# Performance work log

Measured on AMD Instinct MI355X. Metric: run time of the kernel, lower is better.

Reference implementation:

```python
import jax, jax.numpy as jnp
import numpy as np

N = 100000   # nodes
E = 1600000  # edges (avg degree 16)
D = 128      # in = hid = out dim
EPS = 1e-5   # BatchNorm eps


def setup_inputs() -> dict:
    key = jax.random.key(0)
    ks = jax.random.split(key, 14)
    x = jax.random.normal(ks[0], (N, D), dtype=jnp.float32)
    row = jax.random.randint(ks[1], (E,), 0, N, dtype=jnp.int32)
    col = jax.random.randint(ks[2], (E,), 0, N, dtype=jnp.int32)
    edge_weight = jax.random.uniform(ks[3], (E,), dtype=jnp.float32)
    s = 1.0 / np.sqrt(D)
    W0 = jax.random.uniform(ks[4], (D, D), jnp.float32, -s, s)
    b0 = jax.random.uniform(ks[5], (D,), jnp.float32, -s, s)
    W1 = jax.random.uniform(ks[6], (D, D), jnp.float32, -s, s)
    b1 = jax.random.uniform(ks[7], (D,), jnp.float32, -s, s)
    W2 = jax.random.uniform(ks[8], (D, D), jnp.float32, -s, s)
    b2 = jax.random.uniform(ks[9], (D,), jnp.float32, -s, s)
    g0 = jnp.ones((D,), jnp.float32); be0 = jnp.zeros((D,), jnp.float32)
    g1 = jnp.ones((D,), jnp.float32); be1 = jnp.zeros((D,), jnp.float32)
    return {"x": x, "edge_weight": edge_weight,
            "W0": W0, "b0": b0, "g0": g0, "be0": be0,
            "W1": W1, "b1": b1, "g1": g1, "be1": be1,
            "W2": W2, "b2": b2, "row": row, "col": col}


def _spmm(edge_weight, row, col, h):
    # (A_norm @ h) with A in COO: out[r] = sum_e w_e * h[col_e] for row_e == r
    return jax.ops.segment_sum(edge_weight[:, None] * h[col], row, num_segments=N)


def _bn(h, gamma, beta):
    # BatchNorm1d, training-mode stats (biased variance), over the node axis
    m = h.mean(axis=0)
    v = h.var(axis=0)
    return gamma * (h - m) * jax.lax.rsqrt(v + EPS) + beta


def reference(x, edge_weight, W0, b0, g0, be0, W1, b1, g1, be1, W2, b2, row, col):
    # hidden block 1: SpMM(A, Linear(h)) -> BN -> ReLU (dropout p=0)
    h = jax.nn.relu(_bn(_spmm(edge_weight, row, col, x @ W0 + b0), g0, be0))
    # hidden block 2
    h = jax.nn.relu(_bn(_spmm(edge_weight, row, col, h @ W1 + b1), g1, be1))
    # final layer: SpMM(A, Linear(h)), no BN/activation
    return _spmm(edge_weight, row, col, h @ W2 + b2)
```

## Files before the change

### kernel.cpp

```cpp
#include <hip/hip_runtime.h>
#include <cstddef>

#define DD 128
#define EPS 1e-5f

typedef short short8 __attribute__((ext_vector_type(8)));
typedef float float4v __attribute__((ext_vector_type(4)));

__device__ __forceinline__ unsigned short f2bf(float f) {
    union { float f; unsigned int u; } x; x.f = f;
    unsigned int r = x.u + 0x7fffu + ((x.u >> 16) & 1u);
    return (unsigned short)(r >> 16);
}
__device__ __forceinline__ float bfhi2f(unsigned int hi_bits) {
    union { unsigned int u; float f; } x; x.u = hi_bits;
    return x.f;
}


__global__ void hist_kernel(const int* __restrict__ row, int* __restrict__ deg, int E) {
    int e = blockIdx.x * blockDim.x + threadIdx.x;
    if (e < E) atomicAdd(&deg[row[e]], 1);
}

__global__ void scanA_kernel(const int* __restrict__ deg, int* __restrict__ tmp,
                             int* __restrict__ bsum, int n) {
    __shared__ int s[1024];
    int tid = threadIdx.x;
    int gid = blockIdx.x * 1024 + tid;
    int v = (gid < n) ? deg[gid] : 0;
    s[tid] = v;
    __syncthreads();
    for (int off = 1; off < 1024; off <<= 1) {
        int t = s[tid];
        int u = (tid >= off) ? s[tid - off] : 0;
        __syncthreads();
        s[tid] = t + u;
        __syncthreads();
    }
    if (gid < n) tmp[gid] = s[tid];
    if (tid == 1023) bsum[blockIdx.x] = s[1023];
}

__global__ void scanB_kernel(const int* __restrict__ bsum, int* __restrict__ boff,
                             int* __restrict__ row_start, int nb, int n) {
    __shared__ int s[128];
    int tid = threadIdx.x;
    int v = (tid < nb) ? bsum[tid] : 0;
    s[tid] = v;
    __syncthreads();
    for (int off = 1; off < 128; off <<= 1) {
        int t = s[tid];
        int u = (tid >= off) ? s[tid - off] : 0;
        __syncthreads();
        s[tid] = t + u;
        __syncthreads();
    }
    if (tid < nb) boff[tid] = s[tid] - v;
    if (tid == nb - 1) row_start[n] = s[tid];
}

__global__ void scanC_kernel(const int* __restrict__ deg, const int* __restrict__ tmp,
                             const int* __restrict__ boff, int* __restrict__ row_start,
                             int* __restrict__ cursor, int n) {
    int gid = blockIdx.x * 1024 + threadIdx.x;
    if (gid < n) {
        int rs = tmp[gid] - deg[gid] + boff[blockIdx.x];
        row_start[gid] = rs;
        cursor[gid] = rs;
    }
}

#define SCHUNK 2048

__global__ __launch_bounds__(256) void scatter_bucketed_kernel(
    const int* __restrict__ row, const int* __restrict__ col,
    const float* __restrict__ ew, int* __restrict__ cursor,
    unsigned long long* __restrict__ ebuf, int E, unsigned int bmagic) {
    int chunk = blockIdx.x >> 3;
    unsigned int bucket = blockIdx.x & 7;
    int base = chunk * SCHUNK + threadIdx.x;
    #pragma unroll
    for (int i = 0; i < SCHUNK / 256; ++i) {
        int e = base + i * 256;
        if (e < E) {
            int r = row[e];
            if (__umulhi((unsigned int)r, bmagic) == bucket) {
                int p = atomicAdd(&cursor[r], 1);
                unsigned long long pk = (unsigned long long)(unsigned int)col[e]
                                      | ((unsigned long long)__float_as_uint(ew[e]) << 32);
                ebuf[p] = pk;
            }
        }
    }
}


__global__ void convw_kernel(const float* __restrict__ W0, const float* __restrict__ W1,
                             const float* __restrict__ W2, unsigned short* __restrict__ T0,
                             unsigned short* __restrict__ T1, unsigned short* __restrict__ T2) {
    const float* W = (blockIdx.y == 0) ? W0 : (blockIdx.y == 1) ? W1 : W2;
    unsigned short* T = (blockIdx.y == 0) ? T0 : (blockIdx.y == 1) ? T1 : T2;
    int gid = blockIdx.x * 256 + threadIdx.x;
    int k = gid >> 7, n = gid & 127;
    T[n * DD + k] = f2bf(W[k * DD + n]);
}


__global__ __launch_bounds__(256) void gemm_mfma_kernel(
    const float* __restrict__ A, const unsigned short* __restrict__ Wt,
    const float* __restrict__ bias,
    const float* __restrict__ sums, const float* __restrict__ g,
    const float* __restrict__ be,
    int doBN, unsigned short* __restrict__ H, int nrows)
{
    __shared__ unsigned short Asl[64][136];
    __shared__ unsigned short Wsl[128][136];
    __shared__ float scl_s[128], sft_s[128];

    const int tid  = threadIdx.x;
    const int row0 = blockIdx.x * 64;

    if (doBN && tid < 128) {
        float inv_n = 1.0f / (float)nrows;
        float mean = sums[tid] * inv_n;
        float var = sums[128 + tid] * inv_n - mean * mean;
        float rstd = rsqrtf(var + EPS);
        float sc = g[tid] * rstd;
        scl_s[tid] = sc;
        sft_s[tid] = be[tid] - mean * sc;
    }
    if (doBN) __syncthreads();

    for (int i = tid; i < 2048; i += 256) {
        int r = i >> 4, off = (i & 15) * 8;
        *(uint4*)&Wsl[r][off] = *(const uint4*)(Wt + (size_t)r * DD + off);
    }
    for (int i = tid; i < 2048; i += 256) {
        int r = i >> 5, off4 = i & 31;
        int grow = row0 + r;
        float4 v = make_float4(0.f, 0.f, 0.f, 0.f);
        if (grow < nrows)
            v = *(const float4*)(A + (size_t)grow * DD + off4 * 4);
        if (doBN) {
            float4 sc = *(const float4*)&scl_s[off4 * 4];
            float4 sh = *(const float4*)&sft_s[off4 * 4];
            v.x = fmaxf(0.f, v.x * sc.x + sh.x);
            v.y = fmaxf(0.f, v.y * sc.y + sh.y);
            v.z = fmaxf(0.f, v.z * sc.z + sh.z);
            v.w = fmaxf(0.f, v.w * sc.w + sh.w);
        }
        ushort4 p;
        p.x = f2bf(v.x); p.y = f2bf(v.y); p.z = f2bf(v.z); p.w = f2bf(v.w);
        *(ushort4*)&Asl[r][off4 * 4] = p;
    }
    __syncthreads();

    const int w = tid >> 6, lane = tid & 63;
    const int m = lane & 15, q = lane >> 4;

    short8 afr[4];
    #pragma unroll
    for (int c = 0; c < 4; ++c)
        afr[c] = *(const short8*)&Asl[w * 16 + m][c * 32 + q * 8];

    float4v acc[8];
    #pragma unroll
    for (int t = 0; t < 8; ++t) acc[t] = (float4v){0.f, 0.f, 0.f, 0.f};

    #pragma unroll
    for (int t = 0; t < 8; ++t) {
        #pragma unroll
        for (int c = 0; c < 4; ++c) {
            short8 bfr = *(const short8*)&Wsl[t * 16 + m][c * 32 + q * 8];
            acc[t] = __builtin_amdgcn_mfma_f32_16x16x32_bf16(afr[c], bfr, acc[t], 0, 0, 0);
        }
    }

    #pragma unroll
    for (int t = 0; t < 8; ++t) {
        float bv = bias[t * 16 + m];
        #pragma unroll
        for (int i = 0; i < 4; ++i)
            Asl[w * 16 + q * 4 + i][t * 16 + m] = f2bf(acc[t][i] + bv);
    }
    __syncthreads();

    for (int i = tid; i < 1024; i += 256) {
        int r = i >> 4, off = (i & 15) * 8;
        if (row0 + r < nrows)
            *(uint4*)(H + (size_t)(row0 + r) * DD + off) = *(const uint4*)&Asl[r][off];
    }
}


__global__ __launch_bounds__(256) void spmm_bf16_kernel(
    const unsigned short* __restrict__ H, const int* __restrict__ row_start,
    const unsigned long long* __restrict__ ebuf,
    float* __restrict__ S, int N)
{
    int g = threadIdx.x >> 6, lane = threadIdx.x & 63;
    int r = blockIdx.x * 4 + g;
    if (r >= N) return;
    int e0 = row_start[r];
    int e1 = row_start[r + 1];
    float ax = 0.f, ay = 0.f;
    const unsigned short* Hp = H + lane * 2;
    int e = e0;
    for (; e + 3 < e1; e += 4) {
        unsigned long long p0 = __builtin_nontemporal_load(&ebuf[e]);
        unsigned long long p1 = __builtin_nontemporal_load(&ebuf[e + 1]);
        unsigned long long p2 = __builtin_nontemporal_load(&ebuf[e + 2]);
        unsigned long long p3 = __builtin_nontemporal_load(&ebuf[e + 3]);
        unsigned int u0 = *(const unsigned int*)(Hp + (size_t)(unsigned int)p0 * DD);
        unsigned int u1 = *(const unsigned int*)(Hp + (size_t)(unsigned int)p1 * DD);
        unsigned int u2 = *(const unsigned int*)(Hp + (size_t)(unsigned int)p2 * DD);
        unsigned int u3 = *(const unsigned int*)(Hp + (size_t)(unsigned int)p3 * DD);
        float w0 = __uint_as_float((unsigned int)(p0 >> 32));
        float w1 = __uint_as_float((unsigned int)(p1 >> 32));
        float w2 = __uint_as_float((unsigned int)(p2 >> 32));
        float w3 = __uint_as_float((unsigned int)(p3 >> 32));
        ax += w0 * bfhi2f(u0 << 16);
        ay += w0 * bfhi2f(u0 & 0xffff0000u);
        ax += w1 * bfhi2f(u1 << 16);
        ay += w1 * bfhi2f(u1 & 0xffff0000u);
        ax += w2 * bfhi2f(u2 << 16);
        ay += w2 * bfhi2f(u2 & 0xffff0000u);
        ax += w3 * bfhi2f(u3 << 16);
        ay += w3 * bfhi2f(u3 & 0xffff0000u);
    }
    for (; e < e1; ++e) {
        unsigned long long p0 = __builtin_nontemporal_load(&ebuf[e]);
        unsigned int u0 = *(const unsigned int*)(Hp + (size_t)(unsigned int)p0 * DD);
        float w0 = __uint_as_float((unsigned int)(p0 >> 32));
        ax += w0 * bfhi2f(u0 << 16);
        ay += w0 * bfhi2f(u0 & 0xffff0000u);
    }
    float2 o; o.x = ax; o.y = ay;
    *(float2*)(S + (size_t)r * DD + lane * 2) = o;
}


__global__ void bn_stats_kernel(const float* __restrict__ S, float* __restrict__ sums, int n) {
    __shared__ float ls[256], ls2[256];
    int tid = threadIdx.x;
    int c = tid & 127;
    float s = 0.f, s2 = 0.f;
    size_t total = (size_t)n * DD;
    #pragma unroll 8
    for (size_t i = (size_t)blockIdx.x * 256 + tid; i < total; i += (size_t)256 * 256) {
        float v = S[i];
        s += v;
        s2 += v * v;
    }
    ls[tid] = s;
    ls2[tid] = s2;
    __syncthreads();
    if (tid < 128) {
        s  = ls[tid] + ls[tid + 128];
        s2 = ls2[tid] + ls2[tid + 128];
        atomicAdd(&sums[c], s);
        atomicAdd(&sums[128 + c], s2);
    }
}


extern "C" void kernel_launch(void* const* d_in, const int* in_sizes, int n_in,
                              void* d_out, int out_size, void* d_ws, size_t ws_size,
                              hipStream_t stream) {
    const float* x   = (const float*)d_in[0];
    const float* ew  = (const float*)d_in[1];
    const float* W0  = (const float*)d_in[2];
    const float* b0  = (const float*)d_in[3];
    const float* g0  = (const float*)d_in[4];
    const float* be0 = (const float*)d_in[5];
    const float* W1  = (const float*)d_in[6];
    const float* b1  = (const float*)d_in[7];
    const float* g1  = (const float*)d_in[8];
    const float* be1 = (const float*)d_in[9];
    const float* W2  = (const float*)d_in[10];
    const float* b2  = (const float*)d_in[11];
    const int* row   = (const int*)d_in[12];
    const int* col   = (const int*)d_in[13];

    const int N = in_sizes[0] / DD;
    const int E = in_sizes[1];
    float* out = (float*)d_out;

    char* w = (char*)d_ws;
    unsigned short* H   = (unsigned short*)w; w += (size_t)N * DD * 2;
    unsigned long long* ebuf = (unsigned long long*)w; w += (size_t)E * 8;
    unsigned short* Wt0 = (unsigned short*)w; w += DD * DD * 2;
    unsigned short* Wt1 = (unsigned short*)w; w += DD * DD * 2;
    unsigned short* Wt2 = (unsigned short*)w; w += DD * DD * 2;
    float* sums         = (float*)w;          w += 256 * 4;
    int*   deg          = (int*)w;            w += (size_t)N * 4;
    int*   tmp          = (int*)w;            w += (size_t)N * 4;
    int*   cursor       = (int*)w;            w += (size_t)N * 4;
    int*   bsum         = (int*)w;            w += 128 * 4;
    int*   boff         = (int*)w;            w += 128 * 4;
    int*   row_start    = (int*)w;            w += (size_t)(N + 1) * 4;

    unsigned int bmagic = (unsigned int)(((unsigned long long)8 << 32) / (unsigned long long)N);

    hipMemsetAsync(deg, 0, (size_t)N * 4, stream);
    hist_kernel<<<(E + 255) / 256, 256, 0, stream>>>(row, deg, E);
    int NB = (N + 1023) / 1024;
    scanA_kernel<<<NB, 1024, 0, stream>>>(deg, tmp, bsum, N);
    scanB_kernel<<<1, 128, 0, stream>>>(bsum, boff, row_start, NB, N);
    scanC_kernel<<<NB, 1024, 0, stream>>>(deg, tmp, boff, row_start, cursor, N);
    int nchunks = (E + SCHUNK - 1) / SCHUNK;
    scatter_bucketed_kernel<<<nchunks * 8, 256, 0, stream>>>(row, col, ew, cursor, ebuf, E, bmagic);

    convw_kernel<<<dim3(64, 3), 256, 0, stream>>>(W0, W1, W2, Wt0, Wt1, Wt2);

    int gblocks = (N + 63) / 64;
    int sblocks = (N + 3) / 4;

    gemm_mfma_kernel<<<gblocks, 256, 0, stream>>>(x, Wt0, b0, nullptr, nullptr, nullptr, 0, H, N);
    spmm_bf16_kernel<<<sblocks, 256, 0, stream>>>(H, row_start, ebuf, out, N);
    hipMemsetAsync(sums, 0, 256 * 4, stream);
    bn_stats_kernel<<<256, 256, 0, stream>>>(out, sums, N);

    gemm_mfma_kernel<<<gblocks, 256, 0, stream>>>(out, Wt1, b1, sums, g0, be0, 1, H, N);
    spmm_bf16_kernel<<<sblocks, 256, 0, stream>>>(H, row_start, ebuf, out, N);
    hipMemsetAsync(sums, 0, 256 * 4, stream);
    bn_stats_kernel<<<256, 256, 0, stream>>>(out, sums, N);

    gemm_mfma_kernel<<<gblocks, 256, 0, stream>>>(out, Wt2, b2, sums, g1, be1, 1, H, N);
    spmm_bf16_kernel<<<sblocks, 256, 0, stream>>>(H, row_start, ebuf, out, N);
}
```

Baseline: 675.8 us.

## Store intermediate SpMM outputs in bf16 and unroll SpMM gather by eight

The first two SpMM layers now write their outputs as packed bf16 instead of fp32, and the BN statistics and the following GEMM read that bf16 buffer. This halves the traffic for the write, the stats pass and the GEMM input load. The GEMM is split into an fp32-input variant and a bf16-input variant with BN fused. The SpMM inner loop is unrolled to eight gathers in flight. The cost is extra rounding of the pre-BN activations to bf16, which slightly changes the BN statistics and the numerics.

```diff
diff --git a/kernel.cpp b/kernel.cpp
--- a/kernel.cpp
+++ b/kernel.cpp
@@ -107,12 +107,76 @@
 }
 
 
-__global__ __launch_bounds__(256) void gemm_mfma_kernel(
+__global__ __launch_bounds__(256) void gemm_mfma_f32_kernel(
     const float* __restrict__ A, const unsigned short* __restrict__ Wt,
+    const float* __restrict__ bias, unsigned short* __restrict__ H, int nrows)
+{
+    __shared__ unsigned short Asl[64][136];
+    __shared__ unsigned short Wsl[128][136];
+
+    const int tid  = threadIdx.x;
+    const int row0 = blockIdx.x * 64;
+
+    for (int i = tid; i < 2048; i += 256) {
+        int r = i >> 4, off = (i & 15) * 8;
+        *(uint4*)&Wsl[r][off] = *(const uint4*)(Wt + (size_t)r * DD + off);
+    }
+    for (int i = tid; i < 2048; i += 256) {
+        int r = i >> 5, off4 = i & 31;
+        int grow = row0 + r;
+        float4 v = make_float4(0.f, 0.f, 0.f, 0.f);
+        if (grow < nrows)
+            v = *(const float4*)(A + (size_t)grow * DD + off4 * 4);
+        ushort4 p;
+        p.x = f2bf(v.x); p.y = f2bf(v.y); p.z = f2bf(v.z); p.w = f2bf(v.w);
+        *(ushort4*)&Asl[r][off4 * 4] = p;
+    }
+    __syncthreads();
+
+    const int w = tid >> 6, lane = tid & 63;
+    const int m = lane & 15, q = lane >> 4;
+
+    short8 afr[4];
+    #pragma unroll
+    for (int c = 0; c < 4; ++c)
+        afr[c] = *(const short8*)&Asl[w * 16 + m][c * 32 + q * 8];
+
+    float4v acc[8];
+    #pragma unroll
+    for (int t = 0; t < 8; ++t) acc[t] = (float4v){0.f, 0.f, 0.f, 0.f};
+
+    #pragma unroll
+    for (int t = 0; t < 8; ++t) {
+        #pragma unroll
+        for (int c = 0; c < 4; ++c) {
+            short8 bfr = *(const short8*)&Wsl[t * 16 + m][c * 32 + q * 8];
+            acc[t] = __builtin_amdgcn_mfma_f32_16x16x32_bf16(afr[c], bfr, acc[t], 0, 0, 0);
+        }
+    }
+
+    #pragma unroll
+    for (int t = 0; t < 8; ++t) {
+        float bv = bias[t * 16 + m];
+        #pragma unroll
+        for (int i = 0; i < 4; ++i)
+            Asl[w * 16 + q * 4 + i][t * 16 + m] = f2bf(acc[t][i] + bv);
+    }
+    __syncthreads();
+
+    for (int i = tid; i < 1024; i += 256) {
+        int r = i >> 4, off = (i & 15) * 8;
+        if (row0 + r < nrows)
+            *(uint4*)(H + (size_t)(row0 + r) * DD + off) = *(const uint4*)&Asl[r][off];
+    }
+}
+
+
+__global__ __launch_bounds__(256) void gemm_mfma_bf16_kernel(
+    const unsigned int* __restrict__ A, const unsigned short* __restrict__ Wt,
     const float* __restrict__ bias,
     const float* __restrict__ sums, const float* __restrict__ g,
     const float* __restrict__ be,
-    int doBN, unsigned short* __restrict__ H, int nrows)
+    unsigned short* __restrict__ H, int nrows)
 {
     __shared__ unsigned short Asl[64][136];
     __shared__ unsigned short Wsl[128][136];
@@ -121,7 +185,7 @@
     const int tid  = threadIdx.x;
     const int row0 = blockIdx.x * 64;
 
-    if (doBN && tid < 128) {
+    if (tid < 128) {
         float inv_n = 1.0f / (float)nrows;
         float mean = sums[tid] * inv_n;
         float var = sums[128 + tid] * inv_n - mean * mean;
@@ -130,29 +194,31 @@
         scl_s[tid] = sc;
         sft_s[tid] = be[tid] - mean * sc;
     }
-    if (doBN) __syncthreads();
 
     for (int i = tid; i < 2048; i += 256) {
         int r = i >> 4, off = (i & 15) * 8;
         *(uint4*)&Wsl[r][off] = *(const uint4*)(Wt + (size_t)r * DD + off);
     }
-    for (int i = tid; i < 2048; i += 256) {
-        int r = i >> 5, off4 = i & 31;
+    __syncthreads();
+
+    for (int i = tid; i < 1024; i += 256) {
+        int r = i >> 4, ch = (i & 15) * 8;
         int grow = row0 + r;
-        float4 v = make_float4(0.f, 0.f, 0.f, 0.f);
+        uint4 u = make_uint4(0, 0, 0, 0);
         if (grow < nrows)
-            v = *(const float4*)(A + (size_t)grow * DD + off4 * 4);
-        if (doBN) {
-            float4 sc = *(const float4*)&scl_s[off4 * 4];
-            float4 sh = *(const float4*)&sft_s[off4 * 4];
-            v.x = fmaxf(0.f, v.x * sc.x + sh.x);
-            v.y = fmaxf(0.f, v.y * sc.y + sh.y);
-            v.z = fmaxf(0.f, v.z * sc.z + sh.z);
-            v.w = fmaxf(0.f, v.w * sc.w + sh.w);
-        }
-        ushort4 p;
-        p.x = f2bf(v.x); p.y = f2bf(v.y); p.z = f2bf(v.z); p.w = f2bf(v.w);
-        *(ushort4*)&Asl[r][off4 * 4] = p;
+            u = *(const uint4*)(A + (size_t)grow * 64 + (ch >> 1));
+        unsigned int uu[4] = {u.x, u.y, u.z, u.w};
+        unsigned int outp[4];
+        #pragma unroll
+        for (int j = 0; j < 4; ++j) {
+            float vx = bfhi2f(uu[j] << 16);
+            float vy = bfhi2f(uu[j] & 0xffff0000u);
+            int k = ch + j * 2;
+            vx = fmaxf(0.f, vx * scl_s[k] + sft_s[k]);
+            vy = fmaxf(0.f, vy * scl_s[k + 1] + sft_s[k + 1]);
+            outp[j] = (unsigned int)f2bf(vx) | ((unsigned int)f2bf(vy) << 16);
+        }
+        *(uint4*)&Asl[r][ch] = *(const uint4*)outp;
     }
     __syncthreads();
 
@@ -197,37 +263,45 @@
 __global__ __launch_bounds__(256) void spmm_bf16_kernel(
     const unsigned short* __restrict__ H, const int* __restrict__ row_start,
     const unsigned long long* __restrict__ ebuf,
-    float* __restrict__ S, int N)
+    float* __restrict__ Sf, unsigned int* __restrict__ Sb, int writeBF, int N)
 {
     int g = threadIdx.x >> 6, lane = threadIdx.x & 63;
     int r = blockIdx.x * 4 + g;
     if (r >= N) return;
-    int e0 = row_start[r];
-    int e1 = row_start[r + 1];
+    int e0 = row_start[r], e1 = row_start[r + 1];
+    const unsigned short* Hp = H + lane * 2;
     float ax = 0.f, ay = 0.f;
-    const unsigned short* Hp = H + lane * 2;
     int e = e0;
-    for (; e + 3 < e1; e += 4) {
-        unsigned long long p0 = __builtin_nontemporal_load(&ebuf[e]);
-        unsigned long long p1 = __builtin_nontemporal_load(&ebuf[e + 1]);
-        unsigned long long p2 = __builtin_nontemporal_load(&ebuf[e + 2]);
-        unsigned long long p3 = __builtin_nontemporal_load(&ebuf[e + 3]);
-        unsigned int u0 = *(const unsigned int*)(Hp + (size_t)(unsigned int)p0 * DD);
-        unsigned int u1 = *(const unsigned int*)(Hp + (size_t)(unsigned int)p1 * DD);
-        unsigned int u2 = *(const unsigned int*)(Hp + (size_t)(unsigned int)p2 * DD);
-        unsigned int u3 = *(const unsigned int*)(Hp + (size_t)(unsigned int)p3 * DD);
-        float w0 = __uint_as_float((unsigned int)(p0 >> 32));
-        float w1 = __uint_as_float((unsigned int)(p1 >> 32));
-        float w2 = __uint_as_float((unsigned int)(p2 >> 32));
-        float w3 = __uint_as_float((unsigned int)(p3 >> 32));
-        ax += w0 * bfhi2f(u0 << 16);
-        ay += w0 * bfhi2f(u0 & 0xffff0000u);
-        ax += w1 * bfhi2f(u1 << 16);
-        ay += w1 * bfhi2f(u1 & 0xffff0000u);
-        ax += w2 * bfhi2f(u2 << 16);
-        ay += w2 * bfhi2f(u2 & 0xffff0000u);
-        ax += w3 * bfhi2f(u3 << 16);
-        ay += w3 * bfhi2f(u3 & 0xffff0000u);
+    for (; e + 7 < e1; e += 8) {
+        unsigned long long p[8];
+        #pragma unroll
+        for (int j = 0; j < 8; ++j) p[j] = __builtin_nontemporal_load(&ebuf[e + j]);
+        unsigned int u[8];
+        #pragma unroll
+        for (int j = 0; j < 8; ++j)
+            u[j] = *(const unsigned int*)(Hp + (size_t)(unsigned int)p[j] * DD);
+        #pragma unroll
+        for (int j = 0; j < 8; ++j) {
+            float wj = __uint_as_float((unsigned int)(p[j] >> 32));
+            ax += wj * bfhi2f(u[j] << 16);
+            ay += wj * bfhi2f(u[j] & 0xffff0000u);
+        }
+    }
+    if (e + 3 < e1) {
+        unsigned long long p[4];
+        #pragma unroll
+        for (int j = 0; j < 4; ++j) p[j] = __builtin_nontemporal_load(&ebuf[e + j]);
+        unsigned int u[4];
+        #pragma unroll
+        for (int j = 0; j < 4; ++j)
+            u[j] = *(const unsigned int*)(Hp + (size_t)(unsigned int)p[j] * DD);
+        #pragma unroll
+        for (int j = 0; j < 4; ++j) {
+            float wj = __uint_as_float((unsigned int)(p[j] >> 32));
+            ax += wj * bfhi2f(u[j] << 16);
+            ay += wj * bfhi2f(u[j] & 0xffff0000u);
+        }
+        e += 4;
     }
     for (; e < e1; ++e) {
         unsigned long long p0 = __builtin_nontemporal_load(&ebuf[e]);
@@ -236,31 +310,41 @@
         ax += w0 * bfhi2f(u0 << 16);
         ay += w0 * bfhi2f(u0 & 0xffff0000u);
     }
-    float2 o; o.x = ax; o.y = ay;
-    *(float2*)(S + (size_t)r * DD + lane * 2) = o;
-}
-
-
-__global__ void bn_stats_kernel(const float* __restrict__ S, float* __restrict__ sums, int n) {
-    __shared__ float ls[256], ls2[256];
+    if (writeBF) {
+        unsigned int pk = (unsigned int)f2bf(ax) | ((unsigned int)f2bf(ay) << 16);
+        Sb[(size_t)r * 64 + lane] = pk;
+    } else {
+        float2 o; o.x = ax; o.y = ay;
+        *(float2*)(Sf + (size_t)r * DD + lane * 2) = o;
+    }
+}
+
+
+__global__ void bn_stats_bf16_kernel(const unsigned int* __restrict__ Sb,
+                                     float* __restrict__ sums, int n) {
+    __shared__ float lsx[256], lsx2[256], lsy[256], lsy2[256];
     int tid = threadIdx.x;
-    int c = tid & 127;
-    float s = 0.f, s2 = 0.f;
-    size_t total = (size_t)n * DD;
-    #pragma unroll 8
-    for (size_t i = (size_t)blockIdx.x * 256 + tid; i < total; i += (size_t)256 * 256) {
-        float v = S[i];
-        s += v;
-        s2 += v * v;
-    }
-    ls[tid] = s;
-    ls2[tid] = s2;
-    __syncthreads();
-    if (tid < 128) {
-        s  = ls[tid] + ls[tid + 128];
-        s2 = ls2[tid] + ls2[tid + 128];
-        atomicAdd(&sums[c], s);
-        atomicAdd(&sums[128 + c], s2);
+    int c2 = tid & 63;
+    float sx = 0.f, sx2 = 0.f, sy = 0.f, sy2 = 0.f;
+    int total = n * 64;
+    for (int i = blockIdx.x * 256 + tid; i < total; i += 256 * 256) {
+        unsigned int u = Sb[i];
+        float vx = bfhi2f(u << 16);
+        float vy = bfhi2f(u & 0xffff0000u);
+        sx += vx; sx2 += vx * vx;
+        sy += vy; sy2 += vy * vy;
+    }
+    lsx[tid] = sx; lsx2[tid] = sx2; lsy[tid] = sy; lsy2[tid] = sy2;
+    __syncthreads();
+    if (tid < 64) {
+        sx  = lsx[tid]  + lsx[tid + 64]  + lsx[tid + 128]  + lsx[tid + 192];
+        sx2 = lsx2[tid] + lsx2[tid + 64] + lsx2[tid + 128] + lsx2[tid + 192];
+        sy  = lsy[tid]  + lsy[tid + 64]  + lsy[tid + 128]  + lsy[tid + 192];
+        sy2 = lsy2[tid] + lsy2[tid + 64] + lsy2[tid + 128] + lsy2[tid + 192];
+        atomicAdd(&sums[2 * c2], sx);
+        atomicAdd(&sums[2 * c2 + 1], sy);
+        atomicAdd(&sums[128 + 2 * c2], sx2);
+        atomicAdd(&sums[129 + 2 * c2], sy2);
     }
 }
 
@@ -289,6 +373,7 @@
 
     char* w = (char*)d_ws;
     unsigned short* H   = (unsigned short*)w; w += (size_t)N * DD * 2;
+    unsigned int* Sb    = (unsigned int*)w;   w += (size_t)N * 64 * 4;
     unsigned long long* ebuf = (unsigned long long*)w; w += (size_t)E * 8;
     unsigned short* Wt0 = (unsigned short*)w; w += DD * DD * 2;
     unsigned short* Wt1 = (unsigned short*)w; w += DD * DD * 2;
@@ -317,16 +402,16 @@
     int gblocks = (N + 63) / 64;
     int sblocks = (N + 3) / 4;
 
-    gemm_mfma_kernel<<<gblocks, 256, 0, stream>>>(x, Wt0, b0, nullptr, nullptr, nullptr, 0, H, N);
-    spmm_bf16_kernel<<<sblocks, 256, 0, stream>>>(H, row_start, ebuf, out, N);
+    gemm_mfma_f32_kernel<<<gblocks, 256, 0, stream>>>(x, Wt0, b0, H, N);
+    spmm_bf16_kernel<<<sblocks, 256, 0, stream>>>(H, row_start, ebuf, nullptr, Sb, 1, N);
     hipMemsetAsync(sums, 0, 256 * 4, stream);
-    bn_stats_kernel<<<256, 256, 0, stream>>>(out, sums, N);
-
-    gemm_mfma_kernel<<<gblocks, 256, 0, stream>>>(out, Wt1, b1, sums, g0, be0, 1, H, N);
-    spmm_bf16_kernel<<<sblocks, 256, 0, stream>>>(H, row_start, ebuf, out, N);
+    bn_stats_bf16_kernel<<<256, 256, 0, stream>>>(Sb, sums, N);
+
+    gemm_mfma_bf16_kernel<<<gblocks, 256, 0, stream>>>(Sb, Wt1, b1, sums, g0, be0, H, N);
+    spmm_bf16_kernel<<<sblocks, 256, 0, stream>>>(H, row_start, ebuf, nullptr, Sb, 1, N);
     hipMemsetAsync(sums, 0, 256 * 4, stream);
-    bn_stats_kernel<<<256, 256, 0, stream>>>(out, sums, N);
-
-    gemm_mfma_kernel<<<gblocks, 256, 0, stream>>>(out, Wt2, b2, sums, g1, be1, 1, H, N);
-    spmm_bf16_kernel<<<sblocks, 256, 0, stream>>>(H, row_start, ebuf, out, N);
-}
+    bn_stats_bf16_kernel<<<256, 256, 0, stream>>>(Sb, sums, N);
+
+    gemm_mfma_bf16_kernel<<<gblocks, 256, 0, stream>>>(Sb, Wt2, b2, sums, g1, be1, H, N);
+    spmm_bf16_kernel<<<sblocks, 256, 0, stream>>>(H, row_start, ebuf, out, nullptr, 0, N);
+}
```

After: 630.1 us. 1.07x faster.
